# Kernel tuning notes

Hardware: AMD Instinct MI355X
Metric: run time of the kernel (lower is better)

## Reference

```python
import jax, jax.numpy as jnp
import numpy as np
from jax import lax

I = 128   # input_size
H = 128   # recurrent_state_size
T = 2048  # timesteps
N = 256   # parallel envs


def setup_inputs() -> dict:
    key = jax.random.key(0)
    k = jax.random.split(key, 8)
    bound = 1.0 / np.sqrt(H)
    x = jax.random.normal(k[0], (T * N, I), dtype=jnp.float32)
    recurrent_states = jax.random.normal(k[1], (N, H), dtype=jnp.float32)
    recurrent_state_masks = (jax.random.uniform(k[2], (T * N,)) > 0.005).astype(jnp.float32)
    w_ih = jax.random.uniform(k[3], (3 * H, I), minval=-bound, maxval=bound, dtype=jnp.float32)
    w_hh = jax.random.uniform(k[4], (3 * H, H), minval=-bound, maxval=bound, dtype=jnp.float32)
    b_ih = jax.random.uniform(k[5], (3 * H,), minval=-bound, maxval=bound, dtype=jnp.float32)
    b_hh = jax.random.uniform(k[6], (3 * H,), minval=-bound, maxval=bound, dtype=jnp.float32)
    return {"x": x, "recurrent_states": recurrent_states,
            "recurrent_state_masks": recurrent_state_masks,
            "w_ih": w_ih, "w_hh": w_hh, "b_ih": b_ih, "b_hh": b_hh}


def reference(x, recurrent_states, recurrent_state_masks, w_ih, w_hh, b_ih, b_hh):
    n_env, hid = recurrent_states.shape
    t_steps = x.shape[0] // n_env
    xs = x.reshape(t_steps, n_env, -1)                       # [T, N, I]
    masks = recurrent_state_masks.reshape(t_steps, n_env, 1)  # [T, N, 1]
    # input-side gate preactivations, computed once as a big GEMM
    gi = jnp.einsum('tni,gi->tng', xs, w_ih) + b_ih           # [T, N, 3H]

    def step(h, inp):
        gi_t, m_t = inp
        h = h * m_t                                           # episode reset
        gh = jnp.einsum('nh,gh->ng', h, w_hh) + b_hh          # [N, 3H]
        i_r, i_z, i_n = jnp.split(gi_t, 3, axis=-1)
        h_r, h_z, h_n = jnp.split(gh, 3, axis=-1)
        r = jax.nn.sigmoid(i_r + h_r)
        z = jax.nn.sigmoid(i_z + h_z)
        n = jnp.tanh(i_n + r * h_n)
        h_new = (1.0 - z) * n + z * h
        return h_new, h_new

    h_final, outs = lax.scan(step, recurrent_states, (gi, masks))
    return outs.reshape(t_steps * n_env, hid), h_final
```

## Files before the change

### kernel.cpp

```cpp
#include <hip/hip_runtime.h>

#define TSTEPS 2048
#define NENV   256
#define HID    128
#define EPB    16
#define NBLK   (NENV / EPB)
#define NTHREADS 512

#define XP_T_STRIDE (NBLK * 2048)
#define XP_BYTES  ((size_t)TSTEPS * XP_T_STRIDE * 2)

#define LOG2E 1.4426950408889634f

typedef float          floatx4  __attribute__((ext_vector_type(4)));
typedef __bf16         bf16x8   __attribute__((ext_vector_type(8)));
typedef unsigned short ushortx8 __attribute__((ext_vector_type(8)));
typedef unsigned int   uintx4   __attribute__((ext_vector_type(4)));
typedef unsigned int   uintx2   __attribute__((ext_vector_type(2)));

__device__ __forceinline__ unsigned short f2bf(float f) {
    unsigned u = __float_as_uint(f);
    u += 0x7FFFu + ((u >> 16) & 1u);
    return (unsigned short)(u >> 16);
}

__device__ __forceinline__ unsigned cvt_pk_bf16(float a, float b) {
#if __has_builtin(__builtin_amdgcn_cvt_pk_bf16_f32)
    typedef __bf16 bf16x2 __attribute__((ext_vector_type(2)));
    bf16x2 r = __builtin_amdgcn_cvt_pk_bf16_f32(a, b);
    return __builtin_bit_cast(unsigned, r);
#else
    return (unsigned)f2bf(a) | ((unsigned)f2bf(b) << 16);
#endif
}

__device__ __forceinline__ bf16x8 pack8(floatx4 a, floatx4 b) {
    uintx4 u;
    u[0] = cvt_pk_bf16(a[0], a[1]);
    u[1] = cvt_pk_bf16(a[2], a[3]);
    u[2] = cvt_pk_bf16(b[0], b[1]);
    u[3] = cvt_pk_bf16(b[2], b[3]);
    return __builtin_bit_cast(bf16x8, u);
}

__device__ __forceinline__ float fast_rcp(float x) {
#if __has_builtin(__builtin_amdgcn_rcpf)
    return __builtin_amdgcn_rcpf(x);
#else
    return 1.0f / x;
#endif
}
__device__ __forceinline__ float exp2_fast(float x) {
#if __has_builtin(__builtin_amdgcn_exp2f)
    return __builtin_amdgcn_exp2f(x);
#else
    float r; asm("v_exp_f32 %0, %1" : "=v"(r) : "v"(x)); return r;
#endif
}
__device__ __forceinline__ float sigm(float x) {
    return fast_rcp(1.0f + __expf(-x));
}
__device__ __forceinline__ float tanh_fast(float x) {
    return 1.0f - 2.0f * fast_rcp(1.0f + __expf(2.0f * x));
}

__global__ __launch_bounds__(256, 4)
void x_pack(const float* __restrict__ x, unsigned short* __restrict__ xp)
{
    const int tid  = threadIdx.x;
    const int kk   = tid >> 6;
    const int quad = (tid >> 4) & 3;
    const int l15  = tid & 15;
    const int t    = blockIdx.x >> 4;
    const int eb   = blockIdx.x & 15;

    const float* xr = x + (size_t)(t * NENV + eb * EPB + l15) * HID
                        + kk * 32 + quad * 8;
    floatx4 f0 = *(const floatx4*)(xr);
    floatx4 f1 = *(const floatx4*)(xr + 4);
    bf16x8 v = pack8(f0, f1);
    *(bf16x8*)(xp + (size_t)blockIdx.x * 2048 + tid * 8) = v;
}

__global__ __launch_bounds__(NTHREADS, 2)
void gru_scan(const unsigned short* __restrict__ xp,
              const float* __restrict__ h0,
              const float* __restrict__ masks,
              const float* __restrict__ w_ih,
              const float* __restrict__ w_hh,
              const float* __restrict__ b_ih,
              const float* __restrict__ b_hh,
              float* __restrict__ out)
{
    __shared__ unsigned short hbuf[2][EPB][136];

    const int tid  = threadIdx.x;
    const int wv   = tid >> 6;
    const int lane = tid & 63;
    const int quad = lane >> 4;
    const int l15  = lane & 15;
    const int envbase = blockIdx.x * EPB;
    const int j  = wv * 16 + l15;
    const int jb = wv * 16 + quad * 4;

    const float gscale[3] = { -LOG2E, -LOG2E, 2.0f * LOG2E };

    bf16x8 bI[3][4], bH[3][4];
#pragma unroll
    for (int q = 0; q < 3; ++q) {
        const int col = q * HID + j;
        const float s = gscale[q];
#pragma unroll
        for (int kk = 0; kk < 4; ++kk) {
            const int kb = kk * 32 + quad * 8;
            floatx4 f0 = *(const floatx4*)(w_ih + col * HID + kb);
            floatx4 f1 = *(const floatx4*)(w_ih + col * HID + kb + 4);
            bI[q][kk] = pack8(f0 * s, f1 * s);
            floatx4 g0 = *(const floatx4*)(w_hh + col * HID + kb);
            floatx4 g1 = *(const floatx4*)(w_hh + col * HID + kb + 4);
            bH[q][kk] = pack8(g0 * s, g1 * s);
        }
    }
    floatx4 biasRv, biasZv, biasNIv, biasNHv;
    {
        floatx4 bi0 = *(const floatx4*)(b_ih + jb);
        floatx4 bh0 = *(const floatx4*)(b_hh + jb);
        floatx4 bi1 = *(const floatx4*)(b_ih + HID + jb);
        floatx4 bh1 = *(const floatx4*)(b_hh + HID + jb);
        floatx4 bi2 = *(const floatx4*)(b_ih + 2 * HID + jb);
        floatx4 bh2 = *(const floatx4*)(b_hh + 2 * HID + jb);
        biasRv  = (bi0 + bh0) * (-LOG2E);
        biasZv  = (bi1 + bh1) * (-LOG2E);
        biasNIv = bi2 * (2.0f * LOG2E);
        biasNHv = bh2 * (2.0f * LOG2E);
    }

    float hC[4];
    {
        floatx4 h0v = *(const floatx4*)(h0 + (size_t)(envbase + l15) * HID + jb);
        float m0 = masks[envbase + l15];
#pragma unroll
        for (int i = 0; i < 4; ++i) hC[i] = h0v[i] * m0;
        uintx2 w; w[0] = cvt_pk_bf16(hC[0], hC[1]); w[1] = cvt_pk_bf16(hC[2], hC[3]);
        *(uintx2*)&hbuf[0][l15][jb] = w;
    }

    const unsigned short* xbase = xp + (size_t)blockIdx.x * 2048
                                     + quad * 128 + l15 * 8;

    bf16x8 xA[4], xB[4];
#pragma unroll
    for (int kk = 0; kk < 4; ++kk) {
        xA[kk] = __builtin_bit_cast(bf16x8, *(const ushortx8*)(xbase + kk * 512));
        xB[kk] = __builtin_bit_cast(bf16x8, *(const ushortx8*)(xbase + XP_T_STRIDE + kk * 512));
    }
    float mA = masks[(size_t)1 * NENV + envbase + l15];
    float mB = masks[(size_t)2 * NENV + envbase + l15];

    float* const outs = out;
    float* const hfin = out + (size_t)TSTEPS * NENV * HID;

    auto step = [&](int t, int p, bf16x8 (&xc)[4], float& mreg) {
        asm volatile("s_waitcnt lgkmcnt(0)" ::: "memory");
        __builtin_amdgcn_s_barrier();
        __builtin_amdgcn_sched_barrier(0);

        bf16x8 ah[4];
#pragma unroll
        for (int kk = 0; kk < 4; ++kk) {
            ah[kk] = __builtin_bit_cast(bf16x8,
                *(const ushortx8*)&hbuf[p][l15][kk * 32 + quad * 8]);
        }

        floatx4 accR  = biasRv;
        floatx4 accZ  = biasZv;
        floatx4 accNI = biasNIv;
        floatx4 accNH = biasNHv;

#pragma unroll
        for (int kk = 0; kk < 4; ++kk) {
            accR  = __builtin_amdgcn_mfma_f32_16x16x32_bf16(bI[0][kk], xc[kk], accR,  0, 0, 0);
            accZ  = __builtin_amdgcn_mfma_f32_16x16x32_bf16(bI[1][kk], xc[kk], accZ,  0, 0, 0);
            accNI = __builtin_amdgcn_mfma_f32_16x16x32_bf16(bI[2][kk], xc[kk], accNI, 0, 0, 0);
        }

        if (t + 2 < TSTEPS) {
            const unsigned short* xpp = xbase + (size_t)(t + 2) * XP_T_STRIDE;
#pragma unroll
            for (int kk = 0; kk < 4; ++kk)
                xc[kk] = __builtin_bit_cast(bf16x8, *(const ushortx8*)(xpp + kk * 512));
        }
        float mn = mreg;
        mreg = (t + 3 < TSTEPS)
             ? masks[(size_t)(t + 3) * NENV + envbase + l15] : 1.0f;

#pragma unroll
        for (int kk = 0; kk < 4; ++kk) {
            accR  = __builtin_amdgcn_mfma_f32_16x16x32_bf16(bH[0][kk], ah[kk], accR,  0, 0, 0);
            accZ  = __builtin_amdgcn_mfma_f32_16x16x32_bf16(bH[1][kk], ah[kk], accZ,  0, 0, 0);
            accNH = __builtin_amdgcn_mfma_f32_16x16x32_bf16(bH[2][kk], ah[kk], accNH, 0, 0, 0);
        }

        floatx4 hv;
#pragma unroll
        for (int i = 0; i < 4; ++i) {
            float r    = fast_rcp(1.0f + exp2_fast(accR[i]));
            float z    = fast_rcp(1.0f + exp2_fast(accZ[i]));
            float ti   = accNI[i] + r * accNH[i];
            float n    = 1.0f - 2.0f * fast_rcp(1.0f + exp2_fast(ti));
            float hnew = n + z * (hC[i] - n);
            hv[i] = hnew;
            hC[i] = hnew * mn;
        }
        *(floatx4*)(outs + ((size_t)t * NENV + envbase + l15) * HID + jb) = hv;
        uintx2 w; w[0] = cvt_pk_bf16(hC[0], hC[1]); w[1] = cvt_pk_bf16(hC[2], hC[3]);
        *(uintx2*)&hbuf[p ^ 1][l15][jb] = w;
    };

    for (int t = 0; t < TSTEPS; t += 2) {
        step(t,     0, xA, mA);
        step(t + 1, 1, xB, mB);
    }
    floatx4 hf; hf[0] = hC[0]; hf[1] = hC[1]; hf[2] = hC[2]; hf[3] = hC[3];
    *(floatx4*)(hfin + (size_t)(envbase + l15) * HID + jb) = hf;
}

__global__ __launch_bounds__(NTHREADS, 2)
void gru_fused(const float* __restrict__ x,
               const float* __restrict__ h0,
               const float* __restrict__ masks,
               const float* __restrict__ w_ih,
               const float* __restrict__ w_hh,
               const float* __restrict__ b_ih,
               const float* __restrict__ b_hh,
               float* __restrict__ out)
{
    __shared__ unsigned short hbuf[2][EPB][136];

    const int tid  = threadIdx.x;
    const int wv   = tid >> 6;
    const int lane = tid & 63;
    const int quad = lane >> 4;
    const int l15  = lane & 15;
    const int envbase = blockIdx.x * EPB;
    const int j = wv * 16 + l15;

    bf16x8 bI[3][4], bH[3][4];
#pragma unroll
    for (int q = 0; q < 3; ++q) {
        const int col = q * HID + j;
#pragma unroll
        for (int kk = 0; kk < 4; ++kk) {
            const int kb = kk * 32 + quad * 8;
            floatx4 f0 = *(const floatx4*)(w_ih + col * HID + kb);
            floatx4 f1 = *(const floatx4*)(w_ih + col * HID + kb + 4);
            bI[q][kk] = pack8(f0, f1);
            floatx4 g0 = *(const floatx4*)(w_hh + col * HID + kb);
            floatx4 g1 = *(const floatx4*)(w_hh + col * HID + kb + 4);
            bH[q][kk] = pack8(g0, g1);
        }
    }

    const float biasR  = b_ih[j]           + b_hh[j];
    const float biasZ  = b_ih[HID + j]     + b_hh[HID + j];
    const float biasNI = b_ih[2 * HID + j];
    const float biasNH = b_hh[2 * HID + j];

    float hC[4];
    {
        floatx4 m0 = *(const floatx4*)(masks + envbase + quad * 4);
#pragma unroll
        for (int i = 0; i < 4; ++i) {
            const int e = quad * 4 + i;
            float h = h0[(envbase + e) * HID + j] * m0[i];
            hC[i] = h;
            hbuf[0][e][j] = f2bf(h);
        }
    }

    floatx4 xA[8], xB[8];
    {
        const float* xr = x + (size_t)(envbase + l15) * HID;
#pragma unroll
        for (int kk = 0; kk < 4; ++kk) {
            const int kb = kk * 32 + quad * 8;
            xA[2 * kk]     = *(const floatx4*)(xr + kb);
            xA[2 * kk + 1] = *(const floatx4*)(xr + kb + 4);
        }
    }

    float* const outs = out;
    float* const hfin = out + (size_t)TSTEPS * NENV * HID;

    auto step = [&](int t, int p, floatx4 (&xc)[8], floatx4 (&xn)[8]) {
        __syncthreads();
        bf16x8 ah[4];
#pragma unroll
        for (int kk = 0; kk < 4; ++kk) {
            ah[kk] = __builtin_bit_cast(bf16x8,
                *(const ushortx8*)&hbuf[p][l15][kk * 32 + quad * 8]);
        }
        bf16x8 ax[4];
#pragma unroll
        for (int kk = 0; kk < 4; ++kk) ax[kk] = pack8(xc[2 * kk], xc[2 * kk + 1]);

        if (t + 1 < TSTEPS) {
            const float* xr = x + (size_t)((t + 1) * NENV + envbase + l15) * HID;
#pragma unroll
            for (int kk = 0; kk < 4; ++kk) {
                const int kb = kk * 32 + quad * 8;
                xn[2 * kk]     = *(const floatx4*)(xr + kb);
                xn[2 * kk + 1] = *(const floatx4*)(xr + kb + 4);
            }
        }
        floatx4 mn;
        if (t + 1 < TSTEPS) {
            mn = *(const floatx4*)(masks + (size_t)(t + 1) * NENV + envbase + quad * 4);
        } else {
            mn[0] = mn[1] = mn[2] = mn[3] = 1.0f;
        }

        floatx4 accR  = {biasR,  biasR,  biasR,  biasR};
        floatx4 accZ  = {biasZ,  biasZ,  biasZ,  biasZ};
        floatx4 accNI = {biasNI, biasNI, biasNI, biasNI};
        floatx4 accNH = {biasNH, biasNH, biasNH, biasNH};
#pragma unroll
        for (int kk = 0; kk < 4; ++kk) {
            accR  = __builtin_amdgcn_mfma_f32_16x16x32_bf16(ax[kk], bI[0][kk], accR,  0, 0, 0);
            accR  = __builtin_amdgcn_mfma_f32_16x16x32_bf16(ah[kk], bH[0][kk], accR,  0, 0, 0);
            accZ  = __builtin_amdgcn_mfma_f32_16x16x32_bf16(ax[kk], bI[1][kk], accZ,  0, 0, 0);
            accZ  = __builtin_amdgcn_mfma_f32_16x16x32_bf16(ah[kk], bH[1][kk], accZ,  0, 0, 0);
            accNI = __builtin_amdgcn_mfma_f32_16x16x32_bf16(ax[kk], bI[2][kk], accNI, 0, 0, 0);
            accNH = __builtin_amdgcn_mfma_f32_16x16x32_bf16(ah[kk], bH[2][kk], accNH, 0, 0, 0);
        }

#pragma unroll
        for (int i = 0; i < 4; ++i) {
            const int e = quad * 4 + i;
            float r    = sigm(accR[i]);
            float z    = sigm(accZ[i]);
            float n    = tanh_fast(accNI[i] + r * accNH[i]);
            float hnew = n + z * (hC[i] - n);
            outs[((size_t)t * NENV + envbase + e) * HID + j] = hnew;
            if (t == TSTEPS - 1) hfin[(envbase + e) * HID + j] = hnew;
            float hm = hnew * mn[i];
            hC[i] = hm;
            hbuf[p ^ 1][e][j] = f2bf(hm);
        }
    };

    for (int t = 0; t < TSTEPS; t += 2) {
        step(t,     0, xA, xB);
        step(t + 1, 1, xB, xA);
    }
}

extern "C" void kernel_launch(void* const* d_in, const int* in_sizes, int n_in,
                              void* d_out, int out_size, void* d_ws, size_t ws_size,
                              hipStream_t stream) {
    const float* x    = (const float*)d_in[0];
    const float* h0   = (const float*)d_in[1];
    const float* mks  = (const float*)d_in[2];
    const float* w_ih = (const float*)d_in[3];
    const float* w_hh = (const float*)d_in[4];
    const float* b_ih = (const float*)d_in[5];
    const float* b_hh = (const float*)d_in[6];
    (void)in_sizes; (void)n_in; (void)out_size;

    if (ws_size >= XP_BYTES) {
        unsigned short* xp = (unsigned short*)d_ws;
        x_pack<<<dim3(TSTEPS * NBLK), dim3(256), 0, stream>>>(x, xp);
        gru_scan<<<dim3(NBLK), dim3(NTHREADS), 0, stream>>>(xp, h0, mks, w_ih, w_hh,
                                                            b_ih, b_hh, (float*)d_out);
    } else {
        gru_fused<<<dim3(NBLK), dim3(NTHREADS), 0, stream>>>(
            x, h0, mks, w_ih, w_hh, b_ih, b_hh, (float*)d_out);
    }
}
```

Baseline: 1.987 ms.

## Software-pipeline input-side MFMAs one step ahead and coalesce x_pack via LDS

The scan loop now computes the input-projection MFMAs for step t+1 after the recurrent MFMAs of step t, so only the hidden-state GEMM sits on the serial critical path. The x prefetch distance grows to three steps. The x_pack kernel is rewritten to loop over 8 slabs per block, reading contiguous fp32 rows and transposing through a swizzled LDS buffer so both global reads and writes are coalesced. This adds register pressure for the extra accumulators and prefetch buffers, plus LDS barriers in the pack kernel.

```diff
diff --git a/kernel.cpp b/kernel.cpp
--- a/kernel.cpp
+++ b/kernel.cpp
@@ -64,22 +64,29 @@
     return 1.0f - 2.0f * fast_rcp(1.0f + __expf(2.0f * x));
 }
 
-__global__ __launch_bounds__(256, 4)
+__global__ __launch_bounds__(256)
 void x_pack(const float* __restrict__ x, unsigned short* __restrict__ xp)
 {
+    __shared__ uintx4 lds[256];
     const int tid  = threadIdx.x;
     const int kk   = tid >> 6;
     const int quad = (tid >> 4) & 3;
     const int l15  = tid & 15;
-    const int t    = blockIdx.x >> 4;
-    const int eb   = blockIdx.x & 15;
-
-    const float* xr = x + (size_t)(t * NENV + eb * EPB + l15) * HID
-                        + kk * 32 + quad * 8;
-    floatx4 f0 = *(const floatx4*)(xr);
-    floatx4 f1 = *(const floatx4*)(xr + 4);
-    bf16x8 v = pack8(f0, f1);
-    *(bf16x8*)(xp + (size_t)blockIdx.x * 2048 + tid * 8) = v;
+    const int c    = l15 * 16 + kk * 4 + quad;
+    const int wsw  = tid ^ ((tid >> 4) & 7);
+    const int rsw  = c   ^ ((c   >> 4) & 7);
+
+    for (int it = 0; it < 8; ++it) {
+        const size_t slab = (size_t)it * 4096 + blockIdx.x;
+        const float* src = x + slab * 2048;
+        floatx4 f0 = *(const floatx4*)(src + tid * 8);
+        floatx4 f1 = *(const floatx4*)(src + tid * 8 + 4);
+        lds[wsw] = __builtin_bit_cast(uintx4, pack8(f0, f1));
+        __syncthreads();
+        uintx4 v = lds[rsw];
+        *(uintx4*)(xp + slab * 2048 + tid * 8) = v;
+        __syncthreads();
+    }
 }
 
 __global__ __launch_bounds__(NTHREADS, 2)
@@ -154,13 +161,25 @@
         xA[kk] = __builtin_bit_cast(bf16x8, *(const ushortx8*)(xbase + kk * 512));
         xB[kk] = __builtin_bit_cast(bf16x8, *(const ushortx8*)(xbase + XP_T_STRIDE + kk * 512));
     }
+
+    floatx4 xaccR = biasRv, xaccZ = biasZv, xaccNI = biasNIv;
+#pragma unroll
+    for (int kk = 0; kk < 4; ++kk) {
+        xaccR  = __builtin_amdgcn_mfma_f32_16x16x32_bf16(bI[0][kk], xA[kk], xaccR,  0, 0, 0);
+        xaccZ  = __builtin_amdgcn_mfma_f32_16x16x32_bf16(bI[1][kk], xA[kk], xaccZ,  0, 0, 0);
+        xaccNI = __builtin_amdgcn_mfma_f32_16x16x32_bf16(bI[2][kk], xA[kk], xaccNI, 0, 0, 0);
+    }
+#pragma unroll
+    for (int kk = 0; kk < 4; ++kk)
+        xA[kk] = __builtin_bit_cast(bf16x8, *(const ushortx8*)(xbase + 2 * (size_t)XP_T_STRIDE + kk * 512));
+
     float mA = masks[(size_t)1 * NENV + envbase + l15];
     float mB = masks[(size_t)2 * NENV + envbase + l15];
 
     float* const outs = out;
     float* const hfin = out + (size_t)TSTEPS * NENV * HID;
 
-    auto step = [&](int t, int p, bf16x8 (&xc)[4], float& mreg) {
+    auto step = [&](int t, int p, bf16x8 (&xcN)[4], float& mreg) {
         asm volatile("s_waitcnt lgkmcnt(0)" ::: "memory");
         __builtin_amdgcn_s_barrier();
         __builtin_amdgcn_sched_barrier(0);
@@ -172,34 +191,36 @@
                 *(const ushortx8*)&hbuf[p][l15][kk * 32 + quad * 8]);
         }
 
-        floatx4 accR  = biasRv;
-        floatx4 accZ  = biasZv;
-        floatx4 accNI = biasNIv;
+        floatx4 accR  = xaccR;
+        floatx4 accZ  = xaccZ;
+        floatx4 accNI = xaccNI;
         floatx4 accNH = biasNHv;
 
 #pragma unroll
         for (int kk = 0; kk < 4; ++kk) {
-            accR  = __builtin_amdgcn_mfma_f32_16x16x32_bf16(bI[0][kk], xc[kk], accR,  0, 0, 0);
-            accZ  = __builtin_amdgcn_mfma_f32_16x16x32_bf16(bI[1][kk], xc[kk], accZ,  0, 0, 0);
-            accNI = __builtin_amdgcn_mfma_f32_16x16x32_bf16(bI[2][kk], xc[kk], accNI, 0, 0, 0);
-        }
-
-        if (t + 2 < TSTEPS) {
-            const unsigned short* xpp = xbase + (size_t)(t + 2) * XP_T_STRIDE;
+            accR  = __builtin_amdgcn_mfma_f32_16x16x32_bf16(bH[0][kk], ah[kk], accR,  0, 0, 0);
+            accZ  = __builtin_amdgcn_mfma_f32_16x16x32_bf16(bH[1][kk], ah[kk], accZ,  0, 0, 0);
+            accNH = __builtin_amdgcn_mfma_f32_16x16x32_bf16(bH[2][kk], ah[kk], accNH, 0, 0, 0);
+        }
+
+        if (t + 1 < TSTEPS) {
+            xaccR = biasRv; xaccZ = biasZv; xaccNI = biasNIv;
+#pragma unroll
+            for (int kk = 0; kk < 4; ++kk) {
+                xaccR  = __builtin_amdgcn_mfma_f32_16x16x32_bf16(bI[0][kk], xcN[kk], xaccR,  0, 0, 0);
+                xaccZ  = __builtin_amdgcn_mfma_f32_16x16x32_bf16(bI[1][kk], xcN[kk], xaccZ,  0, 0, 0);
+                xaccNI = __builtin_amdgcn_mfma_f32_16x16x32_bf16(bI[2][kk], xcN[kk], xaccNI, 0, 0, 0);
+            }
+        }
+        if (t + 3 < TSTEPS) {
+            const unsigned short* xpp = xbase + (size_t)(t + 3) * XP_T_STRIDE;
 #pragma unroll
             for (int kk = 0; kk < 4; ++kk)
-                xc[kk] = __builtin_bit_cast(bf16x8, *(const ushortx8*)(xpp + kk * 512));
+                xcN[kk] = __builtin_bit_cast(bf16x8, *(const ushortx8*)(xpp + kk * 512));
         }
         float mn = mreg;
         mreg = (t + 3 < TSTEPS)
              ? masks[(size_t)(t + 3) * NENV + envbase + l15] : 1.0f;
-
-#pragma unroll
-        for (int kk = 0; kk < 4; ++kk) {
-            accR  = __builtin_amdgcn_mfma_f32_16x16x32_bf16(bH[0][kk], ah[kk], accR,  0, 0, 0);
-            accZ  = __builtin_amdgcn_mfma_f32_16x16x32_bf16(bH[1][kk], ah[kk], accZ,  0, 0, 0);
-            accNH = __builtin_amdgcn_mfma_f32_16x16x32_bf16(bH[2][kk], ah[kk], accNH, 0, 0, 0);
-        }
 
         floatx4 hv;
 #pragma unroll
@@ -218,8 +239,8 @@
     };
 
     for (int t = 0; t < TSTEPS; t += 2) {
-        step(t,     0, xA, mA);
-        step(t + 1, 1, xB, mB);
+        step(t,     0, xB, mA);
+        step(t + 1, 1, xA, mB);
     }
     floatx4 hf; hf[0] = hC[0]; hf[1] = hC[1]; hf[2] = hC[2]; hf[3] = hC[3];
     *(floatx4*)(hfin + (size_t)(envbase + l15) * HID + jb) = hf;
@@ -369,7 +390,7 @@
 
     if (ws_size >= XP_BYTES) {
         unsigned short* xp = (unsigned short*)d_ws;
-        x_pack<<<dim3(TSTEPS * NBLK), dim3(256), 0, stream>>>(x, xp);
+        x_pack<<<dim3(4096), dim3(256), 0, stream>>>(x, xp);
         gru_scan<<<dim3(NBLK), dim3(NTHREADS), 0, stream>>>(xp, h0, mks, w_ih, w_hh,
                                                             b_ih, b_hh, (float*)d_out);
     } else {
```

New measurement: 2.088 ms. +5.1%, slower.
